# Kernel optimization log

Hardware: AMD Instinct MI355X
Metric: run time of the kernel (lower is better)

The kernel has to match this reference:

```python
import jax, jax.numpy as jnp
import numpy as np

B, N, E, H = 8, 512, 256, 8
DK = E // H
DIST_BAR = (0.3, 0.7, 1e10)  # init dist_bar + [1e10] appended in forward
NEG = -1e10


def setup_inputs() -> dict:
    key = jax.random.key(0)
    ks = jax.random.split(key, 24)
    s = 0.02
    inp = {
        'query': jax.random.normal(ks[0], (B, N, E), jnp.float32),
        'key':   jax.random.normal(ks[1], (B, N, E), jnp.float32),
        'value': jax.random.normal(ks[2], (B, N, E), jnp.float32),
        'dist':  jax.random.uniform(ks[3], (B, N, N), jnp.float32),
        'mask':  jax.random.randint(ks[4], (B, N, N), 0, 2).astype(jnp.int32),
        # 4 linears (q, k, v, out), stored as [in, out] for x @ W
        'Wq': jax.random.normal(ks[5], (E, E)) * s, 'bq': jnp.zeros((E,)),
        'Wk': jax.random.normal(ks[6], (E, E)) * s, 'bk': jnp.zeros((E,)),
        'Wv': jax.random.normal(ks[7], (E, E)) * s, 'bv': jnp.zeros((E,)),
        'Wo': jax.random.normal(ks[8], (E, E)) * s, 'bo': jnp.zeros((E,)),
        # cnn: Conv2d(1,H,1) -> ReLU -> Conv2d(H,H,1); 1x1 convs = per-pixel linear maps
        'cw1': jax.random.normal(ks[9], (H,)) * s,     'cb1': jnp.zeros((H,)),
        'cw2': jax.random.normal(ks[10], (H, H)) * s,  'cb2': jnp.zeros((H,)),
        # scale_linear: Linear(3E, E) -> ReLU -> Linear(E, E)
        'Ws1': jax.random.normal(ks[11], (3 * E, E)) * s, 'bs1': jnp.zeros((E,)),
        'Ws2': jax.random.normal(ks[12], (E, E)) * s,     'bs2': jnp.zeros((E,)),
    }
    return inp


def reference(query, key, value, dist, mask,
              Wq, bq, Wk, bk, Wv, bv, Wo, bo,
              cw1, cb1, cw2, cb2, Ws1, bs1, Ws2, bs2):
    def heads(x, W, b):  # [B,N,E] -> [B,H,N,DK]
        return (x @ W + b).reshape(B, N, H, DK).transpose(0, 2, 1, 3)

    q, k, v = heads(query, Wq, bq), heads(key, Wk, bk), heads(value, Wv, bv)
    d4 = dist[:, None]  # [B,1,N,N]
    # 1x1 conv stack: [B,1,N,N] -> [B,H,N,N]
    c1 = jax.nn.relu(d4 * cw1[None, :, None, None] + cb1[None, :, None, None])
    dist_conv = jnp.einsum('oi,bijk->bojk', cw2, c1) + cb2[None, :, None, None]

    scores = jnp.einsum('bhqd,bhkd->bhqk', q, k) / np.sqrt(DK).astype(np.float32)
    scores = scores * dist_conv
    scores = jnp.where(mask[:, None] == 0, NEG, scores)

    outs = []
    for bar in DIST_BAR:
        dm = d4 < bar                       # [B,1,N,N] bool
        dm = dm.at[:, :, 0, :].set(True).at[:, :, :, 0].set(True)
        s = jnp.where(dm, scores, NEG)
        p = jax.nn.softmax(s, axis=-1)      # [B,H,N,N]
        o = jnp.einsum('bhqk,bhkd->bhqd', p, v)
        o = o.transpose(0, 2, 1, 3).reshape(B, N, E)
        outs.append(o @ Wo + bo)
    x = jnp.concatenate(outs, axis=-1)      # [B,N,3E]
    h1 = jax.nn.relu(x @ Ws1 + bs1)
    return h1 @ Ws2 + bs2                   # [B,N,E]
```

## Files before the change

### kernel.cpp

```cpp
#include <hip/hip_runtime.h>
#include <math.h>

typedef _Float16 h16;
typedef __attribute__((ext_vector_type(4))) _Float16 h16x4;
typedef __attribute__((ext_vector_type(8))) _Float16 h16x8;
typedef __attribute__((ext_vector_type(4))) float f32x4;
typedef unsigned long long u64t;
typedef unsigned int u32t;
typedef unsigned char u8t;

__global__ __launch_bounds__(256) void prep_k(
    const float* __restrict__ Wq, const float* __restrict__ Wk,
    const float* __restrict__ Wv, const float* __restrict__ Ws2,
    const float* __restrict__ Ws1, const float* __restrict__ bo,
    const float* __restrict__ bs1,
    const float* __restrict__ cw1, const float* __restrict__ cb1,
    const float* __restrict__ cw2, const float* __restrict__ cb2,
    const float* __restrict__ Xq, const float* __restrict__ Xk,
    const float* __restrict__ Xv, const float* __restrict__ Wo,
    h16* __restrict__ WT, float* __restrict__ bcombP,
    float* __restrict__ tthr, float* __restrict__ fLUT,
    h16* __restrict__ XHx, h16* __restrict__ XHw)
{
    const int bid = blockIdx.x;
    __shared__ float T[32][33];
    if (bid < 448) {
        const int z = bid >> 6, idx = bid & 63;
        const float* in = (z == 0) ? Wq : (z == 1) ? Wk : (z == 2) ? Wv :
                          (z == 3) ? Ws2 : (Ws1 + (size_t)(z - 4) * 65536);
        h16* out = WT + (size_t)z * 65536;
        const int t = threadIdx.x, tx = t & 31, ty = t >> 5;
        const int r0 = (idx >> 3) * 32, c0 = (idx & 7) * 32;
        #pragma unroll
        for (int i = 0; i < 4; ++i)
            T[ty + i * 8][tx] = in[(size_t)(r0 + ty + i * 8) * 256 + c0 + tx];
        __syncthreads();
        #pragma unroll
        for (int i = 0; i < 4; ++i)
            out[(size_t)(c0 + ty + i * 8) * 256 + r0 + tx] = (h16)T[tx][ty + i * 8];
    } else if (bid < 464) {
        const int z = bid - 448;
        const int j = threadIdx.x;
        float acc = (z == 0) ? bs1[j] : 0.f;
        const int r0 = z * 48;
        #pragma unroll 4
        for (int r = r0; r < r0 + 48; ++r)
            acc = fmaf(bo[r & 255], Ws1[(size_t)r * 256 + j], acc);
        bcombP[z * 256 + j] = acc;
    } else if (bid == 464) {
        const int t = threadIdx.x;
        const float INVS = 0.17677669529663687f;
        float tv[8]; int zu[8];
        #pragma unroll
        for (int u = 0; u < 8; ++u) {
            const float w = cw1[u];
            zu[u] = (w == 0.f) ? 1 : 0;
            tv[u] = zu[u] ? 3.0e38f : (-cb1[u] / w);
        }
        if (t < 8) tthr[t] = tv[t];
        if (t < 72) {
            const int h = t & 7, jj = t >> 3;
            int rank[8];
            #pragma unroll
            for (int u = 0; u < 8; ++u) {
                int rk = 0;
                #pragma unroll
                for (int v = 0; v < 8; ++v)
                    rk += ((tv[v] < tv[u]) || (tv[v] == tv[u] && v < u)) ? 1 : 0;
                rank[u] = rk;
            }
            float slope = 0.f, inter = cb2[h];
            #pragma unroll
            for (int u = 0; u < 8; ++u) {
                const float c2 = cw2[h * 8 + u];
                if (zu[u]) {
                    inter += c2 * fmaxf(cb1[u], 0.f);
                } else {
                    const bool act = (cw1[u] > 0.f) ? (rank[u] < jj) : (rank[u] >= jj);
                    if (act) {
                        slope = fmaf(c2, cw1[u], slope);
                        inter = fmaf(c2, cb1[u], inter);
                    }
                }
            }
            float2 e; e.x = INVS * slope; e.y = INVS * inter;
            ((float2*)fLUT)[jj * 8 + h] = e;
        }
    } else {
        const size_t idx = (size_t)(bid - 465) * 2048 + (size_t)threadIdx.x * 8;
        const float* src; h16* dst;
        if (idx < 3145728) {
            const int z = (int)(idx >> 20);
            src = ((z == 0) ? Xq : (z == 1) ? Xk : Xv) + (idx & 1048575);
            dst = XHx + idx;
        } else {
            src = Wo + (idx - 3145728);
            dst = XHw + (idx - 3145728);
        }
        float4 f0 = *(const float4*)src;
        float4 f1 = *(const float4*)(src + 4);
        h16x8 hv;
        hv[0] = (h16)f0.x; hv[1] = (h16)f0.y; hv[2] = (h16)f0.z; hv[3] = (h16)f0.w;
        hv[4] = (h16)f1.x; hv[5] = (h16)f1.y; hv[6] = (h16)f1.z; hv[7] = (h16)f1.w;
        *(h16x8*)dst = hv;
    }
}

__global__ __launch_bounds__(256) void qkvw_k(
    const h16* __restrict__ XHx, const h16* __restrict__ XHw,
    const h16* __restrict__ WT,
    const float* __restrict__ bq, const float* __restrict__ bk,
    const float* __restrict__ bv,
    h16* __restrict__ qb, h16* __restrict__ kb, h16* __restrict__ vbT,
    h16* __restrict__ WbigT)
{
    const int bid = blockIdx.x;
    const h16* A; const h16* Bt; const float* bias = nullptr;
    int mode, row0, col0, sgm = 0;
    if (bid < 768) {
        const int z = bid >> 8, r = bid & 255;
        row0 = (r & 63) * 64; col0 = (r >> 6) * 64;
        A = XHx + (size_t)z * 1048576;
        Bt = WT + (size_t)z * 65536;
        bias = (z == 0) ? bq : (z == 1) ? bk : bv;
        mode = z;
    } else {
        const int r = bid - 768;
        sgm = r >> 4; const int tt = r & 15;
        row0 = (tt >> 2) * 64; col0 = (tt & 3) * 64;
        A = XHw; Bt = WT + (size_t)(4 + sgm) * 65536; mode = 3;
    }

    __shared__ __align__(16) h16 As[2][64][40];
    __shared__ __align__(16) h16 Bs[2][64][40];
    const int t = threadIdx.x, w = t >> 6, lane = t & 63;
    const int Q = lane >> 4, n = lane & 15;
    const int sr = t >> 2, sc = (t & 3) * 8;

    auto ldA = [&](int k0) -> h16x8 {
        return *(const h16x8*)(A + (size_t)(row0 + sr) * 256 + k0 + sc);
    };
    auto ldB = [&](int k0) -> h16x8 {
        return *(const h16x8*)(Bt + (size_t)(col0 + sr) * 256 + k0 + sc);
    };

    {
        h16x8 a0 = ldA(0), b0 = ldB(0);
        *(h16x8*)&As[0][sr][sc] = a0;
        *(h16x8*)&Bs[0][sr][sc] = b0;
    }
    __syncthreads();

    f32x4 acc4[4];
    #pragma unroll
    for (int c = 0; c < 4; ++c) acc4[c] = (f32x4){0.f, 0.f, 0.f, 0.f};

    for (int it = 0; it < 8; ++it) {
        const int cur = it & 1;
        h16x8 arN, brN;
        if (it < 7) { arN = ldA(32 * (it + 1)); brN = ldB(32 * (it + 1)); }
        h16x8 af = *(const h16x8*)&As[cur][w * 16 + n][Q * 8];
        #pragma unroll
        for (int cg = 0; cg < 4; ++cg) {
            h16x8 bf = *(const h16x8*)&Bs[cur][cg * 16 + n][Q * 8];
            acc4[cg] = __builtin_amdgcn_mfma_f32_16x16x32_f16(af, bf, acc4[cg], 0, 0, 0);
        }
        if (it < 7) {
            *(h16x8*)&As[cur ^ 1][sr][sc] = arN;
            *(h16x8*)&Bs[cur ^ 1][sr][sc] = brN;
        }
        __syncthreads();
    }

    if (mode < 2) {
        h16* out = mode ? kb : qb;
        #pragma unroll
        for (int cg = 0; cg < 4; ++cg) {
            const float bvv = bias[col0 + cg * 16 + n];
            #pragma unroll
            for (int r = 0; r < 4; ++r)
                out[(size_t)(row0 + w * 16 + 4 * Q + r) * 256 + col0 + cg * 16 + n] =
                    (h16)(acc4[cg][r] + bvv);
        }
    } else if (mode == 2) {
        const int bb = row0 >> 9;
        #pragma unroll
        for (int cg = 0; cg < 4; ++cg) {
            const float bvv = bias[col0 + cg * 16 + n];
            const int col = col0 + cg * 16 + n;
            #pragma unroll
            for (int r = 0; r < 4; ++r) {
                const int m = row0 + w * 16 + 4 * Q + r;
                vbT[((size_t)(bb * 256 + col)) * 512 + (m & 511)] = (h16)(acc4[cg][r] + bvv);
            }
        }
    } else {
        #pragma unroll
        for (int cg = 0; cg < 4; ++cg) {
            const int col = col0 + cg * 16 + n;
            #pragma unroll
            for (int r = 0; r < 4; ++r)
                WbigT[(size_t)col * 768 + sgm * 256 + row0 + w * 16 + 4 * Q + r] =
                    (h16)acc4[cg][r];
        }
    }
}

template<int OUT16RELU>
__global__ __launch_bounds__(256) void hgemm32_k(
    const h16* __restrict__ A, const h16* __restrict__ Bt,
    const float* __restrict__ bias, void* __restrict__ outv, int K, int nbp)
{
    __shared__ __align__(16) h16 As[2][32][72];
    __shared__ __align__(16) h16 Bs[2][64][72];
    const int t = threadIdx.x, w = t >> 6, lane = t & 63;
    const int Q = lane >> 4, n = lane & 15;
    const int row0 = blockIdx.x * 32, col0 = blockIdx.y * 64;
    const int r16 = (w & 1) * 16, c32 = (w >> 1) * 32;
    const int asr = t >> 3, asc = (t & 7) * 8;
    const int bsr = t >> 2, bsc = (t & 3) * 16;

    auto ldA = [&](int k0) -> h16x8 {
        return *(const h16x8*)(A + (size_t)(row0 + asr) * K + k0 + asc);
    };
    auto ldB0 = [&](int k0) -> h16x8 {
        return *(const h16x8*)(Bt + (size_t)(col0 + bsr) * K + k0 + bsc);
    };
    auto ldB1 = [&](int k0) -> h16x8 {
        return *(const h16x8*)(Bt + (size_t)(col0 + bsr) * K + k0 + bsc + 8);
    };

    {
        h16x8 a0 = ldA(0), b0 = ldB0(0), b1 = ldB1(0);
        *(h16x8*)&As[0][asr][asc] = a0;
        *(h16x8*)&Bs[0][bsr][bsc] = b0;
        *(h16x8*)&Bs[0][bsr][bsc + 8] = b1;
    }
    __syncthreads();

    f32x4 acc2[2];
    acc2[0] = (f32x4){0.f, 0.f, 0.f, 0.f};
    acc2[1] = (f32x4){0.f, 0.f, 0.f, 0.f};
    const int iters = K >> 6;

    for (int it = 0; it < iters; ++it) {
        const int cur = it & 1;
        h16x8 arN, brN0, brN1;
        if (it + 1 < iters) {
            arN = ldA(64 * (it + 1));
            brN0 = ldB0(64 * (it + 1));
            brN1 = ldB1(64 * (it + 1));
        }
        #pragma unroll
        for (int kh = 0; kh < 2; ++kh) {
            h16x8 af = *(const h16x8*)&As[cur][r16 + n][kh * 32 + Q * 8];
            #pragma unroll
            for (int cg = 0; cg < 2; ++cg) {
                h16x8 bf = *(const h16x8*)&Bs[cur][c32 + cg * 16 + n][kh * 32 + Q * 8];
                acc2[cg] = __builtin_amdgcn_mfma_f32_16x16x32_f16(af, bf, acc2[cg], 0, 0, 0);
            }
        }
        if (it + 1 < iters) {
            *(h16x8*)&As[cur ^ 1][asr][asc] = arN;
            *(h16x8*)&Bs[cur ^ 1][bsr][bsc] = brN0;
            *(h16x8*)&Bs[cur ^ 1][bsr][bsc + 8] = brN1;
        }
        __syncthreads();
    }

    #pragma unroll
    for (int cg = 0; cg < 2; ++cg) {
        const int col = col0 + c32 + cg * 16 + n;
        float bv = bias[col];
        for (int p = 1; p < nbp; ++p) bv += bias[p * 256 + col];
        #pragma unroll
        for (int r = 0; r < 4; ++r) {
            const int row = row0 + r16 + 4 * Q + r;
            if (OUT16RELU)
                ((h16*)outv)[(size_t)row * 256 + col] = (h16)fmaxf(acc2[cg][r] + bv, 0.f);
            else
                ((float*)outv)[(size_t)row * 256 + col] = acc2[cg][r] + bv;
        }
    }
}

__global__ __launch_bounds__(512, 2) void attn_k(
    const h16* __restrict__ qb, const h16* __restrict__ kb,
    const h16* __restrict__ vbT,
    const float* __restrict__ dist, const int* __restrict__ mask,
    const float* __restrict__ tthr, const float* __restrict__ fLUT,
    h16* __restrict__ OB)
{
    const int bx = blockIdx.x, b = bx >> 5, q0 = (bx & 31) * 16;
    const int t = threadIdx.x, w = t >> 6, lane = t & 63;
    const int Q = lane >> 4, n = lane & 15;
    const int h = w;

    __shared__ __align__(16) h16 Dd[2][16][72];
    __shared__ __align__(16) u8t Cd[2][16][72];
    __shared__ __align__(16) h16 Sx[8][16][72];
    __shared__ __align__(8)  float2 lutS[8][9];

    float th[8];
    #pragma unroll
    for (int u = 0; u < 8; ++u) th[u] = tthr[u];
    if (t < 72) lutS[t & 7][t >> 3] = ((const float2*)fLUT)[t];

    const h16x8 aq =
        *(const h16x8*)(qb + ((size_t)(b * 512 + q0 + n)) * 256 + h * 32 + Q * 8);

    const f32x4 z4 = {0.f, 0.f, 0.f, 0.f};
    f32x4 acc[3][2];
    #pragma unroll
    for (int s = 0; s < 3; ++s) { acc[s][0] = z4; acc[s][1] = z4; }
    float mprev = -3e38f;
    float lsum[3] = {0.f, 0.f, 0.f};

    const int scol = lane;

    auto stage = [&](int buf, int kkb, const float* dp, const int* mp) {
        #pragma unroll
        for (int i = 0; i < 2; ++i) {
            const int row = w + 8 * i;
            const float d = dp[i];
            int idx = 0;
            #pragma unroll
            for (int u = 0; u < 8; ++u) idx += (d > th[u]) ? 1 : 0;
            const bool fr = ((q0 + row) == 0) || ((kkb + scol) == 0);
            const bool keep = (mp[i] != 0);
            const u32t code = (keep && (fr || d < 0.3f) ? 1u : 0u)
                            | (keep && (fr || d < 0.7f) ? 2u : 0u)
                            | (keep ? 4u : 0u)
                            | ((u32t)idx << 3);
            Cd[buf][row][scol] = (u8t)code;
            Dd[buf][row][scol] = (h16)d;
        }
    };

    float dv[2]; int mkv[2];
    #pragma unroll
    for (int i = 0; i < 2; ++i) {
        const size_t off = ((size_t)(b * 512 + q0 + w + 8 * i)) * 512 + scol;
        dv[i] = dist[off]; mkv[i] = mask[off];
    }
    h16x8 kf[4], vf[4];
    #pragma unroll
    for (int cg = 0; cg < 4; ++cg)
        kf[cg] = *(const h16x8*)(kb + ((size_t)(b * 512 + cg * 16 + n)) * 256 + h * 32 + Q * 8);
    #pragma unroll
    for (int nh = 0; nh < 2; ++nh)
        #pragma unroll
        for (int k2 = 0; k2 < 2; ++k2)
            vf[nh * 2 + k2] = *(const h16x8*)(
                vbT + ((size_t)((b * 8 + h) * 32 + nh * 16 + n)) * 512 + k2 * 32 + Q * 8);
    stage(0, 0, dv, mkv);
    __syncthreads();

    for (int kc = 0; kc < 8; ++kc) {
        const int cur = kc & 1, kk0 = kc * 64;

        float dN[2]; int mkN[2]; h16x8 kfN[4], vfN[4];
        if (kc < 7) {
            const int kn = kk0 + 64;
            #pragma unroll
            for (int i = 0; i < 2; ++i) {
                const size_t off = ((size_t)(b * 512 + q0 + w + 8 * i)) * 512 + kn + scol;
                dN[i] = dist[off]; mkN[i] = mask[off];
            }
            #pragma unroll
            for (int cg = 0; cg < 4; ++cg)
                kfN[cg] = *(const h16x8*)(
                    kb + ((size_t)(b * 512 + kn + cg * 16 + n)) * 256 + h * 32 + Q * 8);
            #pragma unroll
            for (int nh = 0; nh < 2; ++nh)
                #pragma unroll
                for (int k2 = 0; k2 < 2; ++k2)
                    vfN[nh * 2 + k2] = *(const h16x8*)(
                        vbT + ((size_t)((b * 8 + h) * 32 + nh * 16 + n)) * 512
                            + kn + k2 * 32 + Q * 8);
        }

        f32x4 s4[4];
        #pragma unroll
        for (int cg = 0; cg < 4; ++cg)
            s4[cg] = __builtin_amdgcn_mfma_f32_16x16x32_f16(aq, kf[cg], z4, 0, 0, 0);

        #pragma unroll
        for (int cg = 0; cg < 4; ++cg)
            #pragma unroll
            for (int r = 0; r < 4; ++r)
                Sx[w][4 * Q + r][cg * 16 + n] = (h16)s4[cg][r];
        __builtin_amdgcn_wave_barrier();

        const u64t cd0 = *(const u64t*)&Cd[cur][n][Q * 8];
        const u64t cd1 = *(const u64t*)&Cd[cur][n][32 + Q * 8];
        const h16x8 dd0 = *(const h16x8*)&Dd[cur][n][Q * 8];
        const h16x8 dd1 = *(const h16x8*)&Dd[cur][n][32 + Q * 8];
        float sv[16];
        {
            h16x8 s0 = *(const h16x8*)&Sx[w][n][Q * 8];
            h16x8 s1 = *(const h16x8*)&Sx[w][n][32 + Q * 8];
            #pragma unroll
            for (int i = 0; i < 16; ++i) {
                const u32t byte = (u32t)((i < 8 ? cd0 : cd1) >> (8 * (i & 7))) & 0xFFu;
                const int idx = (int)(byte >> 3);
                const float2 se = lutS[w][idx];
                const float dfi = (float)((i < 8) ? dd0[i & 7] : dd1[i & 7]);
                const float f = fmaf(dfi, se.x, se.y);
                sv[i] = (float)((i < 8) ? s0[i & 7] : s1[i & 7]) * f;
            }
        }
        float cm = -3e38f;
        #pragma unroll
        for (int i = 0; i < 16; ++i) {
            const u32t cc = (u32t)((i < 8 ? cd0 : cd1) >> (8 * (i & 7))) & 7u;
            cm = fmaxf(cm, (cc & 4u) ? sv[i] : -3e38f);
        }
        cm = fmaxf(cm, __shfl_xor(cm, 16));
        cm = fmaxf(cm, __shfl_xor(cm, 32));
        const float mnew = fmaxf(mprev, cm);
        const float alphaA = __expf(mprev - mnew);
        mprev = mnew;

        #pragma unroll
        for (int r = 0; r < 4; ++r) {
            const float aR = __shfl(alphaA, 4 * Q + r);
            #pragma unroll
            for (int s = 0; s < 3; ++s) { acc[s][0][r] *= aR; acc[s][1][r] *= aR; }
        }

        h16x8 pf[3][2];
        float l0 = 0.f, l1 = 0.f, l2 = 0.f;
        #pragma unroll
        for (int i = 0; i < 16; ++i) {
            const u32t cc = (u32t)((i < 8 ? cd0 : cd1) >> (8 * (i & 7))) & 7u;
            const float e = __expf(sv[i] - mnew);
            const float p0 = (cc & 1u) ? e : 0.f;
            const float p1 = (cc & 2u) ? e : 0.f;
            const float p2 = (cc & 4u) ? e : 0.f;
            l0 += p0; l1 += p1; l2 += p2;
            pf[0][i >> 3][i & 7] = (h16)p0;
            pf[1][i >> 3][i & 7] = (h16)p1;
            pf[2][i >> 3][i & 7] = (h16)p2;
        }
        lsum[0] = lsum[0] * alphaA + l0;
        lsum[1] = lsum[1] * alphaA + l1;
        lsum[2] = lsum[2] * alphaA + l2;

        #pragma unroll
        for (int k2 = 0; k2 < 2; ++k2)
            #pragma unroll
            for (int nh = 0; nh < 2; ++nh)
                #pragma unroll
                for (int s = 0; s < 3; ++s)
                    acc[s][nh] = __builtin_amdgcn_mfma_f32_16x16x32_f16(
                        pf[s][k2], vf[nh * 2 + k2], acc[s][nh], 0, 0, 0);

        if (kc < 7) {
            stage(cur ^ 1, kk0 + 64, dN, mkN);
            #pragma unroll
            for (int i = 0; i < 4; ++i) { kf[i] = kfN[i]; vf[i] = vfN[i]; }
        }
        __syncthreads();
    }

    float lrow[3];
    #pragma unroll
    for (int s = 0; s < 3; ++s) {
        float lv = lsum[s];
        lv += __shfl_xor(lv, 16);
        lv += __shfl_xor(lv, 32);
        lrow[s] = lv;
    }
    #pragma unroll
    for (int s = 0; s < 3; ++s) {
        #pragma unroll
        for (int r = 0; r < 4; ++r) {
            const float il = 1.0f / __shfl(lrow[s], 4 * Q + r);
            const size_t row = (size_t)(b * 512 + q0 + 4 * Q + r);
            h16* op = OB + row * 768 + s * 256 + h * 32 + n;
            op[0]  = (h16)(acc[s][0][r] * il);
            op[16] = (h16)(acc[s][1][r] * il);
        }
    }
}

extern "C" void kernel_launch(void* const* d_in, const int* in_sizes, int n_in,
                              void* d_out, int out_size, void* d_ws, size_t ws_size,
                              hipStream_t stream)
{
    const float* query = (const float*)d_in[0];
    const float* key   = (const float*)d_in[1];
    const float* value = (const float*)d_in[2];
    const float* dist  = (const float*)d_in[3];
    const int*   mask  = (const int*)d_in[4];
    const float* Wq = (const float*)d_in[5];  const float* bq = (const float*)d_in[6];
    const float* Wk = (const float*)d_in[7];  const float* bk = (const float*)d_in[8];
    const float* Wv = (const float*)d_in[9];  const float* bv = (const float*)d_in[10];
    const float* Wo = (const float*)d_in[11]; const float* bo = (const float*)d_in[12];
    const float* cw1 = (const float*)d_in[13]; const float* cb1 = (const float*)d_in[14];
    const float* cw2 = (const float*)d_in[15]; const float* cb2 = (const float*)d_in[16];
    const float* Ws1 = (const float*)d_in[17]; const float* bs1 = (const float*)d_in[18];
    const float* Ws2 = (const float*)d_in[19]; const float* bs2 = (const float*)d_in[20];

    h16* qb    = (h16*)d_ws;
    h16* kb    = qb + 1048576;
    h16* vbT   = kb + 1048576;
    h16* OB    = vbT + 1048576;
    h16* h1    = OB + 3145728;
    h16* WT    = h1 + 1048576;
    h16* WbigT = WT + 458752;
    h16* XHw   = WbigT + 196608;
    float* bcombP = (float*)(XHw + 65536);
    float* tthr   = bcombP + 4096;
    float* fLUT   = tthr + 8;
    h16* XHx   = OB;

    prep_k<<<dim3(2033), 256, 0, stream>>>(Wq, Wk, Wv, Ws2, Ws1, bo, bs1,
                                           cw1, cb1, cw2, cb2,
                                           query, key, value, Wo,
                                           WT, bcombP, tthr, fLUT, XHx, XHw);

    qkvw_k<<<dim3(816), 256, 0, stream>>>(XHx, XHw, WT, bq, bk, bv, qb, kb, vbT, WbigT);

    attn_k<<<dim3(256), 512, 0, stream>>>(qb, kb, vbT, dist, mask,
                                          tthr, fLUT, OB);

    hgemm32_k<1><<<dim3(128, 4), 256, 0, stream>>>(OB, WbigT, bcombP, h1, 768, 16);
    hgemm32_k<0><<<dim3(128, 4), 256, 0, stream>>>(h1, WT + 3 * 65536, bs2, d_out, 256, 1);
}
```

Baseline: 160.4 us.

## Fuse all five stages into one cooperative persistent kernel with grid syncs

Replaces the five separate launches (prep, QKV/W GEMM, attention, two output GEMMs) with a single cooperative kernel of 256 blocks of 512 threads. The stages are separated by grid.sync(), and work inside each stage is distributed over tasks per wave or half-block. The aim is to remove per-launch overhead and inter-kernel gaps. In exchange it fixes the grid at 256 blocks for every stage, so the GEMM stages run with fewer concurrent blocks and pay grid-barrier costs, and it falls back to the old launches if the cooperative launch fails.

```diff
diff --git a/kernel.cpp b/kernel.cpp
--- a/kernel.cpp
+++ b/kernel.cpp
@@ -1,5 +1,8 @@
 #include <hip/hip_runtime.h>
+#include <hip/hip_cooperative_groups.h>
 #include <math.h>
+
+namespace cg = cooperative_groups;
 
 typedef _Float16 h16;
 typedef __attribute__((ext_vector_type(4))) _Float16 h16x4;
@@ -8,6 +11,521 @@
 typedef unsigned long long u64t;
 typedef unsigned int u32t;
 typedef unsigned char u8t;
+
+struct Params {
+    const float *Wq, *Wk, *Wv, *Ws2, *Ws1, *bo, *bs1;
+    const float *cw1, *cb1, *cw2, *cb2;
+    const float *Xq, *Xk, *Xv, *Wo, *bq, *bk, *bv, *bs2;
+    const float *dist; const int *mask;
+    h16 *WT, *qb, *kb, *vbT, *OB, *h1, *WbigT, *XHw, *XHx;
+    float *bcombP, *tthr, *fLUT, *outF;
+};
+
+__device__ __forceinline__ void hgemm_half(
+    int tid, u8t* lds, int task,
+    const h16* __restrict__ A, const h16* __restrict__ Bt,
+    const float* __restrict__ bias, void* __restrict__ outv,
+    int K, int nbp, int out16relu)
+{
+    typedef h16 tA[32][72];
+    typedef h16 tB[64][72];
+    tA* As = (tA*)lds;
+    tB* Bs = (tB*)(lds + 9216);
+    const int w = tid >> 6, ln = tid & 63;
+    const int Q = ln >> 4, n = ln & 15;
+    const int row0 = (task >> 2) * 32, col0 = (task & 3) * 64;
+    const int r16 = (w & 1) * 16, c32 = (w >> 1) * 32;
+    const int asr = tid >> 3, asc = (tid & 7) * 8;
+    const int bsr = tid >> 2, bsc = (tid & 3) * 16;
+
+    auto ldA = [&](int k0) -> h16x8 {
+        return *(const h16x8*)(A + (size_t)(row0 + asr) * K + k0 + asc);
+    };
+    auto ldB0 = [&](int k0) -> h16x8 {
+        return *(const h16x8*)(Bt + (size_t)(col0 + bsr) * K + k0 + bsc);
+    };
+    auto ldB1 = [&](int k0) -> h16x8 {
+        return *(const h16x8*)(Bt + (size_t)(col0 + bsr) * K + k0 + bsc + 8);
+    };
+
+    {
+        h16x8 a0 = ldA(0), b0 = ldB0(0), b1 = ldB1(0);
+        *(h16x8*)&As[0][asr][asc] = a0;
+        *(h16x8*)&Bs[0][bsr][bsc] = b0;
+        *(h16x8*)&Bs[0][bsr][bsc + 8] = b1;
+    }
+    __syncthreads();
+
+    f32x4 acc2[2];
+    acc2[0] = (f32x4){0.f, 0.f, 0.f, 0.f};
+    acc2[1] = (f32x4){0.f, 0.f, 0.f, 0.f};
+    const int iters = K >> 6;
+
+    for (int it = 0; it < iters; ++it) {
+        const int cur = it & 1;
+        h16x8 arN, brN0, brN1;
+        if (it + 1 < iters) {
+            arN = ldA(64 * (it + 1));
+            brN0 = ldB0(64 * (it + 1));
+            brN1 = ldB1(64 * (it + 1));
+        }
+        #pragma unroll
+        for (int kh = 0; kh < 2; ++kh) {
+            h16x8 af = *(const h16x8*)&As[cur][r16 + n][kh * 32 + Q * 8];
+            #pragma unroll
+            for (int cg2 = 0; cg2 < 2; ++cg2) {
+                h16x8 bf = *(const h16x8*)&Bs[cur][c32 + cg2 * 16 + n][kh * 32 + Q * 8];
+                acc2[cg2] = __builtin_amdgcn_mfma_f32_16x16x32_f16(af, bf, acc2[cg2], 0, 0, 0);
+            }
+        }
+        if (it + 1 < iters) {
+            *(h16x8*)&As[cur ^ 1][asr][asc] = arN;
+            *(h16x8*)&Bs[cur ^ 1][bsr][bsc] = brN0;
+            *(h16x8*)&Bs[cur ^ 1][bsr][bsc + 8] = brN1;
+        }
+        __syncthreads();
+    }
+
+    #pragma unroll
+    for (int cg2 = 0; cg2 < 2; ++cg2) {
+        const int col = col0 + c32 + cg2 * 16 + n;
+        float bv = bias[col];
+        for (int pp = 1; pp < nbp; ++pp) bv += bias[pp * 256 + col];
+        #pragma unroll
+        for (int r = 0; r < 4; ++r) {
+            const int row = row0 + r16 + 4 * Q + r;
+            if (out16relu)
+                ((h16*)outv)[(size_t)row * 256 + col] = (h16)fmaxf(acc2[cg2][r] + bv, 0.f);
+            else
+                ((float*)outv)[(size_t)row * 256 + col] = acc2[cg2][r] + bv;
+        }
+    }
+}
+
+__global__ __launch_bounds__(512, 2) void mega_k(Params p)
+{
+    __shared__ __align__(16) u8t smem[55296];
+    cg::grid_group grid = cg::this_grid();
+    const int bid = blockIdx.x;
+    const int t = threadIdx.x;
+    const int w8 = t >> 6, lane = t & 63;
+
+    {
+        const int gw = bid * 8 + w8;
+        for (int task = gw; task < 6785; task += 2048) {
+            if (task < 448) {
+                float* T = (float*)(smem + w8 * 4224);
+                const int z = task >> 6, idx = task & 63;
+                const float* in = (z == 0) ? p.Wq : (z == 1) ? p.Wk :
+                                  (z == 2) ? p.Wv : (z == 3) ? p.Ws2 :
+                                  (p.Ws1 + (size_t)(z - 4) * 65536);
+                h16* out = p.WT + (size_t)z * 65536;
+                const int r0 = (idx >> 3) * 32, c0 = (idx & 7) * 32;
+                const int row = lane >> 1, ch = (lane & 1) * 16;
+                const float* ip = in + (size_t)(r0 + row) * 256 + c0 + ch;
+                #pragma unroll
+                for (int j = 0; j < 4; ++j) {
+                    float4 v = *(const float4*)(ip + 4 * j);
+                    float* tr = T + row * 33 + ch + 4 * j;
+                    tr[0] = v.x; tr[1] = v.y; tr[2] = v.z; tr[3] = v.w;
+                }
+                __builtin_amdgcn_wave_barrier();
+                asm volatile("s_waitcnt lgkmcnt(0)" ::: "memory");
+                __builtin_amdgcn_sched_barrier(0);
+                h16 ov[16] __attribute__((aligned(16)));
+                #pragma unroll
+                for (int j = 0; j < 16; ++j) ov[j] = (h16)T[(ch + j) * 33 + row];
+                h16* op = out + (size_t)(c0 + row) * 256 + r0 + ch;
+                *(h16x8*)op = *(h16x8*)&ov[0];
+                *(h16x8*)(op + 8) = *(h16x8*)&ov[8];
+                __builtin_amdgcn_wave_barrier();
+                asm volatile("s_waitcnt lgkmcnt(0)" ::: "memory");
+            } else if (task < 512) {
+                const int wt = task - 448, chunk = wt >> 2;
+                const int col = (wt & 3) * 64 + lane;
+                float acc = (chunk == 0) ? p.bs1[col] : 0.f;
+                const int r0 = chunk * 48;
+                #pragma unroll 4
+                for (int r = r0; r < r0 + 48; ++r)
+                    acc = fmaf(p.bo[r & 255], p.Ws1[(size_t)r * 256 + col], acc);
+                p.bcombP[chunk * 256 + col] = acc;
+            } else if (task == 512) {
+                const float INVS = 0.17677669529663687f;
+                float tv[8]; int zu[8];
+                #pragma unroll
+                for (int u = 0; u < 8; ++u) {
+                    const float w = p.cw1[u];
+                    zu[u] = (w == 0.f) ? 1 : 0;
+                    tv[u] = zu[u] ? 3.0e38f : (-p.cb1[u] / w);
+                }
+                if (lane < 8) p.tthr[lane] = tv[lane];
+                #pragma unroll
+                for (int ee = 0; ee < 2; ++ee) {
+                    const int e = lane + 64 * ee;
+                    if (e < 72) {
+                        const int h = e & 7, jj = e >> 3;
+                        int rank[8];
+                        #pragma unroll
+                        for (int u = 0; u < 8; ++u) {
+                            int rk = 0;
+                            #pragma unroll
+                            for (int v = 0; v < 8; ++v)
+                                rk += ((tv[v] < tv[u]) || (tv[v] == tv[u] && v < u)) ? 1 : 0;
+                            rank[u] = rk;
+                        }
+                        float slope = 0.f, inter = p.cb2[h];
+                        #pragma unroll
+                        for (int u = 0; u < 8; ++u) {
+                            const float c2 = p.cw2[h * 8 + u];
+                            if (zu[u]) {
+                                inter += c2 * fmaxf(p.cb1[u], 0.f);
+                            } else {
+                                const bool act = (p.cw1[u] > 0.f) ? (rank[u] < jj) : (rank[u] >= jj);
+                                if (act) {
+                                    slope = fmaf(c2, p.cw1[u], slope);
+                                    inter = fmaf(c2, p.cb1[u], inter);
+                                }
+                            }
+                        }
+                        float2 ev; ev.x = INVS * slope; ev.y = INVS * inter;
+                        ((float2*)p.fLUT)[jj * 8 + h] = ev;
+                    }
+                }
+            } else {
+                const size_t basei = (size_t)(task - 513) * 512 + (size_t)lane * 8;
+                const float* src; h16* dst;
+                if (basei < 3145728) {
+                    const int z = (int)(basei >> 20);
+                    src = ((z == 0) ? p.Xq : (z == 1) ? p.Xk : p.Xv) + (basei & 1048575);
+                    dst = p.XHx + basei;
+                } else {
+                    src = p.Wo + (basei - 3145728);
+                    dst = p.XHw + (basei - 3145728);
+                }
+                float4 f0 = *(const float4*)src;
+                float4 f1 = *(const float4*)(src + 4);
+                h16x8 hv;
+                hv[0] = (h16)f0.x; hv[1] = (h16)f0.y; hv[2] = (h16)f0.z; hv[3] = (h16)f0.w;
+                hv[4] = (h16)f1.x; hv[5] = (h16)f1.y; hv[6] = (h16)f1.z; hv[7] = (h16)f1.w;
+                *(h16x8*)dst = hv;
+            }
+        }
+    }
+    grid.sync();
+
+    {
+        const int half = t >> 8, tid = t & 255;
+        u8t* lds = smem + half * 20480;
+        typedef h16 qtile[64][40];
+        qtile* As = (qtile*)lds;
+        qtile* Bs = (qtile*)(lds + 10240);
+        const int wq = tid >> 6, lq = tid & 63;
+        const int Q = lq >> 4, n = lq & 15;
+        const int sr = tid >> 2, sc = (tid & 3) * 8;
+
+        for (int base = 0; base < 816; base += 512) {
+            const int task = base + bid * 2 + half;
+            const bool valid = task < 816;
+            int mode = -1, row0, col0, sgm = 0;
+            const h16 *A = p.XHx, *Bt = p.WT; const float* bias = p.bq;
+            if (valid) {
+                if (task < 768) {
+                    const int z = task >> 8, r = task & 255;
+                    row0 = (r & 63) * 64; col0 = (r >> 6) * 64;
+                    A = p.XHx + (size_t)z * 1048576;
+                    Bt = p.WT + (size_t)z * 65536;
+                    bias = (z == 0) ? p.bq : (z == 1) ? p.bk : p.bv;
+                    mode = z;
+                } else {
+                    const int r = task - 768;
+                    sgm = r >> 4; const int tt2 = r & 15;
+                    row0 = (tt2 >> 2) * 64; col0 = (tt2 & 3) * 64;
+                    A = p.XHw; Bt = p.WT + (size_t)(4 + sgm) * 65536; mode = 3;
+                }
+            } else {
+                const int r = task & 255;
+                row0 = (r & 63) * 64; col0 = (r >> 6) * 64;
+            }
+
+            auto ldA = [&](int k0) -> h16x8 {
+                return *(const h16x8*)(A + (size_t)(row0 + sr) * 256 + k0 + sc);
+            };
+            auto ldB = [&](int k0) -> h16x8 {
+                return *(const h16x8*)(Bt + (size_t)(col0 + sr) * 256 + k0 + sc);
+            };
+
+            {
+                h16x8 a0 = ldA(0), b0 = ldB(0);
+                *(h16x8*)&As[0][sr][sc] = a0;
+                *(h16x8*)&Bs[0][sr][sc] = b0;
+            }
+            __syncthreads();
+
+            f32x4 acc4[4];
+            #pragma unroll
+            for (int c = 0; c < 4; ++c) acc4[c] = (f32x4){0.f, 0.f, 0.f, 0.f};
+
+            for (int it = 0; it < 8; ++it) {
+                const int cur = it & 1;
+                h16x8 arN, brN;
+                if (it < 7) { arN = ldA(32 * (it + 1)); brN = ldB(32 * (it + 1)); }
+                h16x8 af = *(const h16x8*)&As[cur][wq * 16 + n][Q * 8];
+                #pragma unroll
+                for (int cg2 = 0; cg2 < 4; ++cg2) {
+                    h16x8 bf = *(const h16x8*)&Bs[cur][cg2 * 16 + n][Q * 8];
+                    acc4[cg2] = __builtin_amdgcn_mfma_f32_16x16x32_f16(af, bf, acc4[cg2], 0, 0, 0);
+                }
+                if (it < 7) {
+                    *(h16x8*)&As[cur ^ 1][sr][sc] = arN;
+                    *(h16x8*)&Bs[cur ^ 1][sr][sc] = brN;
+                }
+                __syncthreads();
+            }
+
+            if (mode == 0 || mode == 1) {
+                h16* out = mode ? p.kb : p.qb;
+                #pragma unroll
+                for (int cg2 = 0; cg2 < 4; ++cg2) {
+                    const float bvv = bias[col0 + cg2 * 16 + n];
+                    #pragma unroll
+                    for (int r = 0; r < 4; ++r)
+                        out[(size_t)(row0 + wq * 16 + 4 * Q + r) * 256 + col0 + cg2 * 16 + n] =
+                            (h16)(acc4[cg2][r] + bvv);
+                }
+            } else if (mode == 2) {
+                const int bb = row0 >> 9;
+                #pragma unroll
+                for (int cg2 = 0; cg2 < 4; ++cg2) {
+                    const float bvv = bias[col0 + cg2 * 16 + n];
+                    const int col = col0 + cg2 * 16 + n;
+                    #pragma unroll
+                    for (int r = 0; r < 4; ++r) {
+                        const int m = row0 + wq * 16 + 4 * Q + r;
+                        p.vbT[((size_t)(bb * 256 + col)) * 512 + (m & 511)] =
+                            (h16)(acc4[cg2][r] + bvv);
+                    }
+                }
+            } else if (mode == 3) {
+                #pragma unroll
+                for (int cg2 = 0; cg2 < 4; ++cg2) {
+                    const int col = col0 + cg2 * 16 + n;
+                    #pragma unroll
+                    for (int r = 0; r < 4; ++r)
+                        p.WbigT[(size_t)col * 768 + sgm * 256 + row0 + wq * 16 + 4 * Q + r] =
+                            (h16)acc4[cg2][r];
+                }
+            }
+        }
+    }
+    grid.sync();
+
+    {
+        const int b = bid >> 5, q0 = (bid & 31) * 16;
+        const int w = w8, Q = lane >> 4, n = lane & 15;
+        const int h = w;
+        h16 (*Dd)[16][72] = (h16(*)[16][72])(smem);
+        u8t (*Cd)[16][72] = (u8t(*)[16][72])(smem + 4608);
+        h16 (*Sx)[16][72] = (h16(*)[16][72])(smem + 6912);
+        float2 (*lutS)[9] = (float2(*)[9])(smem + 25344);
+
+        float th[8];
+        #pragma unroll
+        for (int u = 0; u < 8; ++u) th[u] = p.tthr[u];
+        if (t < 72) lutS[t & 7][t >> 3] = ((const float2*)p.fLUT)[t];
+
+        const h16x8 aq =
+            *(const h16x8*)(p.qb + ((size_t)(b * 512 + q0 + n)) * 256 + h * 32 + Q * 8);
+
+        const f32x4 z4 = {0.f, 0.f, 0.f, 0.f};
+        f32x4 acc[3][2];
+        #pragma unroll
+        for (int s = 0; s < 3; ++s) { acc[s][0] = z4; acc[s][1] = z4; }
+        float mprev = -3e38f;
+        float lsum[3] = {0.f, 0.f, 0.f};
+
+        const int scol = lane;
+
+        auto stage = [&](int buf, int kkb, const float* dp, const int* mp) {
+            #pragma unroll
+            for (int i = 0; i < 2; ++i) {
+                const int row = w + 8 * i;
+                const float d = dp[i];
+                int idx = 0;
+                #pragma unroll
+                for (int u = 0; u < 8; ++u) idx += (d > th[u]) ? 1 : 0;
+                const bool fr = ((q0 + row) == 0) || ((kkb + scol) == 0);
+                const bool keep = (mp[i] != 0);
+                const u32t code = (keep && (fr || d < 0.3f) ? 1u : 0u)
+                                | (keep && (fr || d < 0.7f) ? 2u : 0u)
+                                | (keep ? 4u : 0u)
+                                | ((u32t)idx << 3);
+                Cd[buf][row][scol] = (u8t)code;
+                Dd[buf][row][scol] = (h16)d;
+            }
+        };
+
+        float dv[2]; int mkv[2];
+        #pragma unroll
+        for (int i = 0; i < 2; ++i) {
+            const size_t off = ((size_t)(b * 512 + q0 + w + 8 * i)) * 512 + scol;
+            dv[i] = p.dist[off]; mkv[i] = p.mask[off];
+        }
+        h16x8 kf[4], vf[4];
+        #pragma unroll
+        for (int cg2 = 0; cg2 < 4; ++cg2)
+            kf[cg2] = *(const h16x8*)(p.kb + ((size_t)(b * 512 + cg2 * 16 + n)) * 256 + h * 32 + Q * 8);
+        #pragma unroll
+        for (int nh = 0; nh < 2; ++nh)
+            #pragma unroll
+            for (int k2 = 0; k2 < 2; ++k2)
+                vf[nh * 2 + k2] = *(const h16x8*)(
+                    p.vbT + ((size_t)((b * 8 + h) * 32 + nh * 16 + n)) * 512 + k2 * 32 + Q * 8);
+        stage(0, 0, dv, mkv);
+        __syncthreads();
+
+        for (int kc = 0; kc < 8; ++kc) {
+            const int cur = kc & 1, kk0 = kc * 64;
+
+            float dN[2]; int mkN[2]; h16x8 kfN[4], vfN[4];
+            if (kc < 7) {
+                const int kn = kk0 + 64;
+                #pragma unroll
+                for (int i = 0; i < 2; ++i) {
+                    const size_t off = ((size_t)(b * 512 + q0 + w + 8 * i)) * 512 + kn + scol;
+                    dN[i] = p.dist[off]; mkN[i] = p.mask[off];
+                }
+                #pragma unroll
+                for (int cg2 = 0; cg2 < 4; ++cg2)
+                    kfN[cg2] = *(const h16x8*)(
+                        p.kb + ((size_t)(b * 512 + kn + cg2 * 16 + n)) * 256 + h * 32 + Q * 8);
+                #pragma unroll
+                for (int nh = 0; nh < 2; ++nh)
+                    #pragma unroll
+                    for (int k2 = 0; k2 < 2; ++k2)
+                        vfN[nh * 2 + k2] = *(const h16x8*)(
+                            p.vbT + ((size_t)((b * 8 + h) * 32 + nh * 16 + n)) * 512
+                                + kn + k2 * 32 + Q * 8);
+            }
+
+            f32x4 s4[4];
+            #pragma unroll
+            for (int cg2 = 0; cg2 < 4; ++cg2)
+                s4[cg2] = __builtin_amdgcn_mfma_f32_16x16x32_f16(aq, kf[cg2], z4, 0, 0, 0);
+
+            #pragma unroll
+            for (int cg2 = 0; cg2 < 4; ++cg2)
+                #pragma unroll
+                for (int r = 0; r < 4; ++r)
+                    Sx[w][4 * Q + r][cg2 * 16 + n] = (h16)s4[cg2][r];
+            __builtin_amdgcn_wave_barrier();
+
+            const u64t cd0 = *(const u64t*)&Cd[cur][n][Q * 8];
+            const u64t cd1 = *(const u64t*)&Cd[cur][n][32 + Q * 8];
+            const h16x8 dd0 = *(const h16x8*)&Dd[cur][n][Q * 8];
+            const h16x8 dd1 = *(const h16x8*)&Dd[cur][n][32 + Q * 8];
+            float sv[16];
+            {
+                h16x8 s0 = *(const h16x8*)&Sx[w][n][Q * 8];
+                h16x8 s1 = *(const h16x8*)&Sx[w][n][32 + Q * 8];
+                #pragma unroll
+                for (int i = 0; i < 16; ++i) {
+                    const u32t byte = (u32t)((i < 8 ? cd0 : cd1) >> (8 * (i & 7))) & 0xFFu;
+                    const int idx = (int)(byte >> 3);
+                    const float2 se = lutS[w][idx];
+                    const float dfi = (float)((i < 8) ? dd0[i & 7] : dd1[i & 7]);
+                    const float f = fmaf(dfi, se.x, se.y);
+                    sv[i] = (float)((i < 8) ? s0[i & 7] : s1[i & 7]) * f;
+                }
+            }
+            float cm = -3e38f;
+            #pragma unroll
+            for (int i = 0; i < 16; ++i) {
+                const u32t cc = (u32t)((i < 8 ? cd0 : cd1) >> (8 * (i & 7))) & 7u;
+                cm = fmaxf(cm, (cc & 4u) ? sv[i] : -3e38f);
+            }
+            cm = fmaxf(cm, __shfl_xor(cm, 16));
+            cm = fmaxf(cm, __shfl_xor(cm, 32));
+            const float mnew = fmaxf(mprev, cm);
+            const float alphaA = __expf(mprev - mnew);
+            mprev = mnew;
+
+            #pragma unroll
+            for (int r = 0; r < 4; ++r) {
+                const float aR = __shfl(alphaA, 4 * Q + r);
+                #pragma unroll
+                for (int s = 0; s < 3; ++s) { acc[s][0][r] *= aR; acc[s][1][r] *= aR; }
+            }
+
+            h16x8 pf[3][2];
+            float l0 = 0.f, l1 = 0.f, l2 = 0.f;
+            #pragma unroll
+            for (int i = 0; i < 16; ++i) {
+                const u32t cc = (u32t)((i < 8 ? cd0 : cd1) >> (8 * (i & 7))) & 7u;
+                const float e = __expf(sv[i] - mnew);
+                const float p0 = (cc & 1u) ? e : 0.f;
+                const float p1 = (cc & 2u) ? e : 0.f;
+                const float p2 = (cc & 4u) ? e : 0.f;
+                l0 += p0; l1 += p1; l2 += p2;
+                pf[0][i >> 3][i & 7] = (h16)p0;
+                pf[1][i >> 3][i & 7] = (h16)p1;
+                pf[2][i >> 3][i & 7] = (h16)p2;
+            }
+            lsum[0] = lsum[0] * alphaA + l0;
+            lsum[1] = lsum[1] * alphaA + l1;
+            lsum[2] = lsum[2] * alphaA + l2;
+
+            #pragma unroll
+            for (int k2 = 0; k2 < 2; ++k2)
+                #pragma unroll
+                for (int nh = 0; nh < 2; ++nh)
+                    #pragma unroll
+                    for (int s = 0; s < 3; ++s)
+                        acc[s][nh] = __builtin_amdgcn_mfma_f32_16x16x32_f16(
+                            pf[s][k2], vf[nh * 2 + k2], acc[s][nh], 0, 0, 0);
+
+            if (kc < 7) {
+                stage(cur ^ 1, kk0 + 64, dN, mkN);
+                #pragma unroll
+                for (int i = 0; i < 4; ++i) { kf[i] = kfN[i]; vf[i] = vfN[i]; }
+            }
+            __syncthreads();
+        }
+
+        float lrow[3];
+        #pragma unroll
+        for (int s = 0; s < 3; ++s) {
+            float lv = lsum[s];
+            lv += __shfl_xor(lv, 16);
+            lv += __shfl_xor(lv, 32);
+            lrow[s] = lv;
+        }
+        #pragma unroll
+        for (int s = 0; s < 3; ++s) {
+            #pragma unroll
+            for (int r = 0; r < 4; ++r) {
+                const float il = 1.0f / __shfl(lrow[s], 4 * Q + r);
+                const size_t row = (size_t)(b * 512 + q0 + 4 * Q + r);
+                h16* op = p.OB + row * 768 + s * 256 + h * 32 + n;
+                op[0]  = (h16)(acc[s][0][r] * il);
+                op[16] = (h16)(acc[s][1][r] * il);
+            }
+        }
+    }
+    grid.sync();
+
+    {
+        const int half = t >> 8, tid = t & 255;
+        u8t* lds = smem + half * 27648;
+        hgemm_half(tid, lds, bid * 2 + half, p.OB, p.WbigT, p.bcombP, p.h1, 768, 16, 1);
+    }
+    grid.sync();
+
+    {
+        const int half = t >> 8, tid = t & 255;
+        u8t* lds = smem + half * 27648;
+        hgemm_half(tid, lds, bid * 2 + half, p.h1, p.WT + 3 * 65536, p.bs2, p.outF, 256, 1, 0);
+    }
+}
 
 __global__ __launch_bounds__(256) void prep_k(
     const float* __restrict__ Wq, const float* __restrict__ Wk,
@@ -161,9 +679,9 @@
         if (it < 7) { arN = ldA(32 * (it + 1)); brN = ldB(32 * (it + 1)); }
         h16x8 af = *(const h16x8*)&As[cur][w * 16 + n][Q * 8];
         #pragma unroll
-        for (int cg = 0; cg < 4; ++cg) {
-            h16x8 bf = *(const h16x8*)&Bs[cur][cg * 16 + n][Q * 8];
-            acc4[cg] = __builtin_amdgcn_mfma_f32_16x16x32_f16(af, bf, acc4[cg], 0, 0, 0);
+        for (int cg2 = 0; cg2 < 4; ++cg2) {
+            h16x8 bf = *(const h16x8*)&Bs[cur][cg2 * 16 + n][Q * 8];
+            acc4[cg2] = __builtin_amdgcn_mfma_f32_16x16x32_f16(af, bf, acc4[cg2], 0, 0, 0);
         }
         if (it < 7) {
             *(h16x8*)&As[cur ^ 1][sr][sc] = arN;
@@ -175,33 +693,33 @@
     if (mode < 2) {
         h16* out = mode ? kb : qb;
         #pragma unroll
-        for (int cg = 0; cg < 4; ++cg) {
-            const float bvv = bias[col0 + cg * 16 + n];
+        for (int cg2 = 0; cg2 < 4; ++cg2) {
+            const float bvv = bias[col0 + cg2 * 16 + n];
             #pragma unroll
             for (int r = 0; r < 4; ++r)
-                out[(size_t)(row0 + w * 16 + 4 * Q + r) * 256 + col0 + cg * 16 + n] =
-                    (h16)(acc4[cg][r] + bvv);
+                out[(size_t)(row0 + w * 16 + 4 * Q + r) * 256 + col0 + cg2 * 16 + n] =
+                    (h16)(acc4[cg2][r] + bvv);
         }
     } else if (mode == 2) {
         const int bb = row0 >> 9;
         #pragma unroll
-        for (int cg = 0; cg < 4; ++cg) {
-            const float bvv = bias[col0 + cg * 16 + n];
-            const int col = col0 + cg * 16 + n;
+        for (int cg2 = 0; cg2 < 4; ++cg2) {
+            const float bvv = bias[col0 + cg2 * 16 + n];
+            const int col = col0 + cg2 * 16 + n;
             #pragma unroll
             for (int r = 0; r < 4; ++r) {
                 const int m = row0 + w * 16 + 4 * Q + r;
-                vbT[((size_t)(bb * 256 + col)) * 512 + (m & 511)] = (h16)(acc4[cg][r] + bvv);
+                vbT[((size_t)(bb * 256 + col)) * 512 + (m & 511)] = (h16)(acc4[cg2][r] + bvv);
             }
         }
     } else {
         #pragma unroll
-        for (int cg = 0; cg < 4; ++cg) {
-            const int col = col0 + cg * 16 + n;
+        for (int cg2 = 0; cg2 < 4; ++cg2) {
+            const int col = col0 + cg2 * 16 + n;
             #pragma unroll
             for (int r = 0; r < 4; ++r)
                 WbigT[(size_t)col * 768 + sgm * 256 + row0 + w * 16 + 4 * Q + r] =
-                    (h16)acc4[cg][r];
+                    (h16)acc4[cg2][r];
         }
     }
 }
@@ -211,77 +729,9 @@
     const h16* __restrict__ A, const h16* __restrict__ Bt,
     const float* __restrict__ bias, void* __restrict__ outv, int K, int nbp)
 {
-    __shared__ __align__(16) h16 As[2][32][72];
-    __shared__ __align__(16) h16 Bs[2][64][72];
-    const int t = threadIdx.x, w = t >> 6, lane = t & 63;
-    const int Q = lane >> 4, n = lane & 15;
-    const int row0 = blockIdx.x * 32, col0 = blockIdx.y * 64;
-    const int r16 = (w & 1) * 16, c32 = (w >> 1) * 32;
-    const int asr = t >> 3, asc = (t & 7) * 8;
-    const int bsr = t >> 2, bsc = (t & 3) * 16;
-
-    auto ldA = [&](int k0) -> h16x8 {
-        return *(const h16x8*)(A + (size_t)(row0 + asr) * K + k0 + asc);
-    };
-    auto ldB0 = [&](int k0) -> h16x8 {
-        return *(const h16x8*)(Bt + (size_t)(col0 + bsr) * K + k0 + bsc);
-    };
-    auto ldB1 = [&](int k0) -> h16x8 {
-        return *(const h16x8*)(Bt + (size_t)(col0 + bsr) * K + k0 + bsc + 8);
-    };
-
-    {
-        h16x8 a0 = ldA(0), b0 = ldB0(0), b1 = ldB1(0);
-        *(h16x8*)&As[0][asr][asc] = a0;
-        *(h16x8*)&Bs[0][bsr][bsc] = b0;
-        *(h16x8*)&Bs[0][bsr][bsc + 8] = b1;
-    }
-    __syncthreads();
-
-    f32x4 acc2[2];
-    acc2[0] = (f32x4){0.f, 0.f, 0.f, 0.f};
-    acc2[1] = (f32x4){0.f, 0.f, 0.f, 0.f};
-    const int iters = K >> 6;
-
-    for (int it = 0; it < iters; ++it) {
-        const int cur = it & 1;
-        h16x8 arN, brN0, brN1;
-        if (it + 1 < iters) {
-            arN = ldA(64 * (it + 1));
-            brN0 = ldB0(64 * (it + 1));
-            brN1 = ldB1(64 * (it + 1));
-        }
-        #pragma unroll
-        for (int kh = 0; kh < 2; ++kh) {
-            h16x8 af = *(const h16x8*)&As[cur][r16 + n][kh * 32 + Q * 8];
-            #pragma unroll
-            for (int cg = 0; cg < 2; ++cg) {
-                h16x8 bf = *(const h16x8*)&Bs[cur][c32 + cg * 16 + n][kh * 32 + Q * 8];
-                acc2[cg] = __builtin_amdgcn_mfma_f32_16x16x32_f16(af, bf, acc2[cg], 0, 0, 0);
-            }
-        }
-        if (it + 1 < iters) {
-            *(h16x8*)&As[cur ^ 1][asr][asc] = arN;
-            *(h16x8*)&Bs[cur ^ 1][bsr][bsc] = brN0;
-            *(h16x8*)&Bs[cur ^ 1][bsr][bsc + 8] = brN1;
-        }
-        __syncthreads();
-    }
-
-    #pragma unroll
-    for (int cg = 0; cg < 2; ++cg) {
-        const int col = col0 + c32 + cg * 16 + n;
-        float bv = bias[col];
-        for (int p = 1; p < nbp; ++p) bv += bias[p * 256 + col];
-        #pragma unroll
-        for (int r = 0; r < 4; ++r) {
-            const int row = row0 + r16 + 4 * Q + r;
-            if (OUT16RELU)
-                ((h16*)outv)[(size_t)row * 256 + col] = (h16)fmaxf(acc2[cg][r] + bv, 0.f);
-            else
-                ((float*)outv)[(size_t)row * 256 + col] = acc2[cg][r] + bv;
-        }
-    }
+    __shared__ __align__(16) u8t lds[27648];
+    const int task = blockIdx.x * 4 + blockIdx.y;
+    hgemm_half(threadIdx.x, lds, task, A, Bt, bias, outv, K, nbp, OUT16RELU);
 }
 
 __global__ __launch_bounds__(512, 2) void attn_k(
@@ -345,8 +795,8 @@
     }
     h16x8 kf[4], vf[4];
     #pragma unroll
-    for (int cg = 0; cg < 4; ++cg)
-        kf[cg] = *(const h16x8*)(kb + ((size_t)(b * 512 + cg * 16 + n)) * 256 + h * 32 + Q * 8);
+    for (int cg2 = 0; cg2 < 4; ++cg2)
+        kf[cg2] = *(const h16x8*)(kb + ((size_t)(b * 512 + cg2 * 16 + n)) * 256 + h * 32 + Q * 8);
     #pragma unroll
     for (int nh = 0; nh < 2; ++nh)
         #pragma unroll
@@ -368,9 +818,9 @@
                 dN[i] = dist[off]; mkN[i] = mask[off];
             }
             #pragma unroll
-            for (int cg = 0; cg < 4; ++cg)
-                kfN[cg] = *(const h16x8*)(
-                    kb + ((size_t)(b * 512 + kn + cg * 16 + n)) * 256 + h * 32 + Q * 8);
+            for (int cg2 = 0; cg2 < 4; ++cg2)
+                kfN[cg2] = *(const h16x8*)(
+                    kb + ((size_t)(b * 512 + kn + cg2 * 16 + n)) * 256 + h * 32 + Q * 8);
             #pragma unroll
             for (int nh = 0; nh < 2; ++nh)
                 #pragma unroll
@@ -382,14 +832,14 @@
 
         f32x4 s4[4];
         #pragma unroll
-        for (int cg = 0; cg < 4; ++cg)
-            s4[cg] = __builtin_amdgcn_mfma_f32_16x16x32_f16(aq, kf[cg], z4, 0, 0, 0);
-
-        #pragma unroll
-        for (int cg = 0; cg < 4; ++cg)
+        for (int cg2 = 0; cg2 < 4; ++cg2)
+            s4[cg2] = __builtin_amdgcn_mfma_f32_16x16x32_f16(aq, kf[cg2], z4, 0, 0, 0);
+
+        #pragma unroll
+        for (int cg2 = 0; cg2 < 4; ++cg2)
             #pragma unroll
             for (int r = 0; r < 4; ++r)
-                Sx[w][4 * Q + r][cg * 16 + n] = (h16)s4[cg][r];
+                Sx[w][4 * Q + r][cg2 * 16 + n] = (h16)s4[cg2][r];
         __builtin_amdgcn_wave_barrier();
 
         const u64t cd0 = *(const u64t*)&Cd[cur][n][Q * 8];
@@ -516,16 +966,32 @@
     float* fLUT   = tthr + 8;
     h16* XHx   = OB;
 
-    prep_k<<<dim3(2033), 256, 0, stream>>>(Wq, Wk, Wv, Ws2, Ws1, bo, bs1,
-                                           cw1, cb1, cw2, cb2,
-                                           query, key, value, Wo,
-                                           WT, bcombP, tthr, fLUT, XHx, XHw);
-
-    qkvw_k<<<dim3(816), 256, 0, stream>>>(XHx, XHw, WT, bq, bk, bv, qb, kb, vbT, WbigT);
-
-    attn_k<<<dim3(256), 512, 0, stream>>>(qb, kb, vbT, dist, mask,
-                                          tthr, fLUT, OB);
-
-    hgemm32_k<1><<<dim3(128, 4), 256, 0, stream>>>(OB, WbigT, bcombP, h1, 768, 16);
-    hgemm32_k<0><<<dim3(128, 4), 256, 0, stream>>>(h1, WT + 3 * 65536, bs2, d_out, 256, 1);
+    Params prm;
+    prm.Wq = Wq; prm.Wk = Wk; prm.Wv = Wv; prm.Ws2 = Ws2; prm.Ws1 = Ws1;
+    prm.bo = bo; prm.bs1 = bs1;
+    prm.cw1 = cw1; prm.cb1 = cb1; prm.cw2 = cw2; prm.cb2 = cb2;
+    prm.Xq = query; prm.Xk = key; prm.Xv = value; prm.Wo = Wo;
+    prm.bq = bq; prm.bk = bk; prm.bv = bv; prm.bs2 = bs2;
+    prm.dist = dist; prm.mask = mask;
+    prm.WT = WT; prm.qb = qb; prm.kb = kb; prm.vbT = vbT; prm.OB = OB;
+    prm.h1 = h1; prm.WbigT = WbigT; prm.XHw = XHw; prm.XHx = XHx;
+    prm.bcombP = bcombP; prm.tthr = tthr; prm.fLUT = fLUT;
+    prm.outF = (float*)d_out;
+
+    void* kargs[] = { (void*)&prm };
+    hipError_t err = hipLaunchCooperativeKernel(
+        (void*)mega_k, dim3(256), dim3(512), kargs, 0, stream);
+
+    if (err != hipSuccess) {
+        prep_k<<<dim3(2033), 256, 0, stream>>>(Wq, Wk, Wv, Ws2, Ws1, bo, bs1,
+                                               cw1, cb1, cw2, cb2,
+                                               query, key, value, Wo,
+                                               WT, bcombP, tthr, fLUT, XHx, XHw);
+        qkvw_k<<<dim3(816), 256, 0, stream>>>(XHx, XHw, WT, bq, bk, bv,
+                                              qb, kb, vbT, WbigT);
+        attn_k<<<dim3(256), 512, 0, stream>>>(qb, kb, vbT, dist, mask,
+                                              tthr, fLUT, OB);
+        hgemm32_k<1><<<dim3(128, 4), 256, 0, stream>>>(OB, WbigT, bcombP, h1, 768, 16);
+        hgemm32_k<0><<<dim3(128, 4), 256, 0, stream>>>(h1, WT + 3 * 65536, bs2, d_out, 256, 1);
+    }
 }
```

Result: slower. 333.9 us (+108.2%).
